# Kernel tuning notes

Measured on AMD Instinct MI355X. Metric: run time of the kernel, lower is better.

## Reference

```python
import jax, jax.numpy as jnp
import numpy as np

NQ = 64
BIG = 1e10

FILTERS = np.array([[1,0,0,1,0,0,1,0,0],
                    [0,0,0,0,0,0,1,1,1],
                    [0,0,1,0,0,1,0,0,1],
                    [1,1,1,0,0,0,0,0,0],
                    [0,0,0,1,0,0,1,1,0],
                    [0,0,0,0,0,1,0,1,1],
                    [0,1,1,0,0,1,0,0,0],
                    [1,1,0,1,0,0,0,0,0]], dtype=np.float32).reshape(8,1,3,3)


def _conv2d(x, k):
    return jax.lax.conv_general_dilated(x, k, (1,1), 'SAME',
                                        dimension_numbers=('NCHW','OIHW','NCHW'))


def _maxpool3(x):  # 3x3 stride-1 maxpool, pad=1 (pads with -inf like torch)
    return jax.lax.reduce_window(x, -jnp.inf, jax.lax.max, (1,1,3,3), (1,1,1,1), 'SAME')


def setup_inputs() -> dict:
    key = jax.random.key(0)
    ks = jax.random.split(key, 5)
    b, h, w = 2, 240, 320
    n = 2 * h * w  # 153600 points
    fx = fy = 300.0
    cx, cy = w / 2.0, h / 2.0
    z  = jax.random.uniform(ks[0], (b, n), minval=1.0, maxval=10.0)
    u  = jax.random.uniform(ks[1], (b, n), minval=0.0, maxval=float(w))
    v  = jax.random.uniform(ks[2], (b, n), minval=0.0, maxval=float(h))
    xw = (u - cx) / fx * z
    yw = (v - cy) / fy * z
    rgb = jax.random.uniform(ks[3], (b, 3, n))
    pp = jnp.concatenate([xw[:, None], yw[:, None], z[:, None],
                          jnp.ones((b, 1, n), jnp.float32), rgb], axis=1)  # [b,7,n]
    conf = jax.random.uniform(ks[4], (b, n))
    pose_w2c = jnp.tile(jnp.eye(4, dtype=jnp.float32)[None], (b, 1, 1))
    K = jnp.tile(jnp.array([[fx, 0, cx], [0, fy, cy], [0, 0, 1.0]], jnp.float32)[None], (b, 1, 1))
    filters = jnp.asarray(FILTERS)
    return {"pp": pp, "conf": conf, "pose_w2c": pose_w2c, "K": K,
            "filters": filters, "h": h, "w": w}


def reference(pp, conf, pose_w2c, K, filters, h, w,
              znear=0.1, zfar=1000.0, conf_thresh=0.0):
    b, _, n = pp.shape
    # world -> camera (wsz=1 so the hi-res pool is identity)
    pc = jnp.einsum('bij,bjn->bin', pose_w2c, pp[:, :4])          # [b,4,n]
    z  = jnp.abs(pc[:, 2])                                        # [b,n]
    xc = pc[:, 0] * K[:, 0, 0][:, None] / z + K[:, 0, 2][:, None]
    yc = pc[:, 1] * K[:, 1, 1][:, None] / z + K[:, 1, 2][:, None]
    x = jnp.round(xc).astype(jnp.int32)
    y = jnp.round(yc).astype(jnp.int32)
    oob = ((x < 0) | (x >= w) | (y < 0) | (y >= h) |
           (z < znear) | (z > zfar) | (conf <= conf_thresh))
    # inverse-depth quantization bounds over valid points only
    inv_lo = 1.0 / jnp.where(oob, 1e-10, z)   # oob -> 1e10, drops out of min
    inv_hi = 1.0 / jnp.where(oob, BIG, z)     # oob -> 1e-10, drops out of max
    dmin = jnp.min(inv_lo, axis=-1, keepdims=True)
    dmax = jnp.max(inv_hi, axis=-1, keepdims=True)
    do = ((inv_hi - dmin) / (dmax - dmin) * (NQ - 1)).astype(jnp.int32)  # [b,n]

    # scatter points into [b, NQ, h, w] z-buffer bins (drop invalid)
    size = b * NQ * h * w
    bidx = jnp.arange(b, dtype=jnp.int32)[:, None]
    idx = ((bidx * NQ + do) * h + y) * w + x
    idx = jnp.where(oob, size, idx).reshape(-1)   # 'size' is out of bounds -> dropped
    zf = z.astype(jnp.float32).reshape(-1)
    dmap = jnp.zeros((size,), jnp.float32).at[idx].set(zf, mode='drop').reshape(b, NQ, h, w)
    cmap = jnp.full((size,), -1.0, jnp.float32).at[idx].set(conf.reshape(-1), mode='drop').reshape(b, NQ, h, w)
    rgb_pts = pp[:, 4:].transpose(0, 2, 1).reshape(-1, 3).astype(jnp.float32)
    rgb = jnp.zeros((size, 3), jnp.float32).at[idx].set(rgb_pts, mode='drop').reshape(b, NQ, h, w, 3)

    # z-buffer composite: nearest non-empty bin per pixel
    dmap = jnp.where(dmap <= 0, BIG, dmap)
    min_idx = jnp.argmin(dmap, axis=1)                             # [b,h,w]
    dflat = jnp.min(dmap, axis=1)
    dflat = jnp.where(dflat >= BIG, 0.0, dflat)
    cflat = jnp.take_along_axis(cmap, min_idx[:, None], axis=1)[:, 0]
    cflat = jnp.maximum(cflat, 0.0)                                # cmap_[cmap_<0]=0
    rflat = jnp.take_along_axis(rgb, min_idx[:, None, :, :, None], axis=1)[:, 0]  # [b,h,w,3]

    # vertical flip (torch.flip over h)
    depths = dflat[:, ::-1][:, None]                               # [b,1,h,w]
    confs  = cflat[:, ::-1][:, None]
    rgbs   = jnp.transpose(rflat[:, ::-1], (0, 3, 1, 2))           # [b,3,h,w]

    # hole filling: 2 iterations of oriented-filter tests + 3x3 max pooling
    ones_k = jnp.ones((1, 1, 3, 3), jnp.float32)
    for _ in range(2):
        tofill = (_conv2d(depths, ones_k) > 0) & (depths <= 0)
        o = _conv2d(depths, filters)                               # [b,8,h,w]
        fill = (jnp.abs(jnp.prod(o, axis=1, keepdims=True)) > 1e-10) & tofill
        f = fill.astype(jnp.float32)
        depths = depths * (1 - f) + f * _maxpool3(depths)
        confs  = confs  * (1 - f) + f * _maxpool3(confs)
        rgbs   = rgbs   * (1 - f) + f * _maxpool3(rgbs)
    return depths, confs, rgbs
```

## Files before the change

### kernel.cpp

```cpp
#include <hip/hip_runtime.h>
#include <stdint.h>

#define NQ 64
#define ZNEAR 0.1f
#define ZFAR 1000.0f
#define FT 16

__device__ __forceinline__ float wave_min_f(float v) {
    #pragma unroll
    for (int off = 1; off < 64; off <<= 1)
        v = fminf(v, __shfl_xor(v, off, 64));
    return v;
}
__device__ __forceinline__ float wave_max_f(float v) {
    #pragma unroll
    for (int off = 1; off < 64; off <<= 1)
        v = fmaxf(v, __shfl_xor(v, off, 64));
    return v;
}

__global__ void k_project(const float* __restrict__ pp, const float* __restrict__ conf,
                          const float* __restrict__ pose, const float* __restrict__ Km,
                          const int* __restrict__ hp, const int* __restrict__ wp,
                          int B, int n,
                          float* __restrict__ zbuf, unsigned* __restrict__ packed,
                          float* __restrict__ pmin, float* __restrict__ pmax, int nBlk) {
    int bb = blockIdx.y;
    int i = blockIdx.x * blockDim.x + threadIdx.x;
    int h = *hp, w = *wp;
    float inv_lo = INFINITY;
    float inv_hi = 0.0f;
    if (i < n) {
        const float* P  = pose + (size_t)bb * 16;
        const float* km = Km   + (size_t)bb * 9;
        const float* pb = pp   + (size_t)bb * 7 * n;
        float X  = pb[0 * (size_t)n + i];
        float Y  = pb[1 * (size_t)n + i];
        float Z  = pb[2 * (size_t)n + i];
        float Wc = pb[3 * (size_t)n + i];
        float pc0 = P[0] * X + P[1] * Y + P[2]  * Z + P[3]  * Wc;
        float pc1 = P[4] * X + P[5] * Y + P[6]  * Z + P[7]  * Wc;
        float pc2 = P[8] * X + P[9] * Y + P[10] * Z + P[11] * Wc;
        float z = fabsf(pc2);
        float xc = pc0 * km[0] / z + km[2];
        float yc = pc1 * km[4] / z + km[5];
        float xr = rintf(xc);
        float yr = rintf(yc);
        float cf = conf[(size_t)bb * n + i];
        bool valid = (xr >= 0.0f) && (xr <= (float)(w - 1)) &&
                     (yr >= 0.0f) && (yr <= (float)(h - 1)) &&
                     (z >= ZNEAR) && (z <= ZFAR) && (cf > 0.0f);
        unsigned px = valid ? (unsigned)(int)xr : 0u;
        unsigned py = valid ? (unsigned)(int)yr : 0u;
        zbuf[(size_t)bb * n + i] = z;
        packed[(size_t)bb * n + i] = (valid ? 0x80000000u : 0u) | px | (py << 12);
        inv_lo = valid ? (1.0f / z) : (1.0f / 1e-10f);
        inv_hi = valid ? (1.0f / z) : (1.0f / 1e10f);
    }
    __shared__ float smin[4], smax[4];
    float wmin = wave_min_f(inv_lo);
    float wmax = wave_max_f(inv_hi);
    int lane = threadIdx.x & 63, wid = threadIdx.x >> 6;
    if (lane == 0) { smin[wid] = wmin; smax[wid] = wmax; }
    __syncthreads();
    if (threadIdx.x == 0) {
        pmin[(size_t)bb * nBlk + blockIdx.x] = fminf(fminf(smin[0], smin[1]), fminf(smin[2], smin[3]));
        pmax[(size_t)bb * nBlk + blockIdx.x] = fmaxf(fmaxf(smax[0], smax[1]), fmaxf(smax[2], smax[3]));
    }
}

__global__ void k_minmax(const float* __restrict__ pmin, const float* __restrict__ pmax,
                         int B, int nBlk, float* __restrict__ dminb, float* __restrict__ dmaxb) {
    __shared__ float smin[4], smax[4];
    for (int bb = 0; bb < B; ++bb) {
        float lmin = INFINITY, lmax = 0.0f;
        for (int k = threadIdx.x; k < nBlk; k += blockDim.x) {
            lmin = fminf(lmin, pmin[(size_t)bb * nBlk + k]);
            lmax = fmaxf(lmax, pmax[(size_t)bb * nBlk + k]);
        }
        lmin = wave_min_f(lmin);
        lmax = wave_max_f(lmax);
        int lane = threadIdx.x & 63, wid = threadIdx.x >> 6;
        if (lane == 0) { smin[wid] = lmin; smax[wid] = lmax; }
        __syncthreads();
        if (threadIdx.x == 0) {
            dminb[bb] = fminf(fminf(smin[0], smin[1]), fminf(smin[2], smin[3]));
            dmaxb[bb] = fmaxf(fmaxf(smax[0], smax[1]), fmaxf(smax[2], smax[3]));
        }
        __syncthreads();
    }
}

__global__ void k_scatter(const float* __restrict__ zbuf, const unsigned* __restrict__ packed,
                          const float* __restrict__ dminb, const float* __restrict__ dmaxb,
                          const int* __restrict__ hp, const int* __restrict__ wp,
                          int B, int n, unsigned* __restrict__ pixwin) {
    int p = blockIdx.x * blockDim.x + threadIdx.x;
    if (p >= B * n) return;
    unsigned pk = packed[p];
    if (!(pk & 0x80000000u)) return;
    int bb = p / n;
    int i = p - bb * n;
    float inv = 1.0f / zbuf[p];
    float dlo = dminb[bb], dhi = dmaxb[bb];
    int dq = (int)((inv - dlo) / (dhi - dlo) * (float)(NQ - 1));
    int h = *hp, w = *wp;
    int x = (int)(pk & 0xFFFu);
    int y = (int)((pk >> 12) & 0xFFFu);
    unsigned key = ((unsigned)dq << 20) | (unsigned)(i + 1);
    atomicMax(&pixwin[(size_t)bb * h * w + (size_t)y * w + x], key);
}

__global__ void k_resolve(const float* __restrict__ pp, const float* __restrict__ conf,
                          const float* __restrict__ zbuf, const unsigned* __restrict__ pixwin,
                          const int* __restrict__ hp, const int* __restrict__ wp,
                          int B, int n, float* __restrict__ field, int pixTot) {
    int q = blockIdx.x * blockDim.x + threadIdx.x;
    if (q >= pixTot) return;
    int h = *hp, w = *wp;
    int hw = h * w;
    int bb = q / hw;
    int rem = q - bb * hw;
    int y = rem / w;
    int x = rem - y * w;
    unsigned key = pixwin[q];
    float dz = 0.0f, dc = 0.0f, r0 = 0.0f, r1 = 0.0f, r2 = 0.0f;
    if (key) {
        int i = (int)(key & 0xFFFFFu) - 1;
        size_t p = (size_t)bb * n + i;
        dz = zbuf[p];
        dc = conf[p];
        r0 = pp[((size_t)bb * 7 + 4) * n + i];
        r1 = pp[((size_t)bb * 7 + 5) * n + i];
        r2 = pp[((size_t)bb * 7 + 6) * n + i];
    }
    int fy = h - 1 - y;
    size_t o = (size_t)bb * hw + (size_t)fy * w + x;
    field[o] = dz;
    field[(size_t)pixTot + o] = dc;
    size_t rb = 2 * (size_t)pixTot;
    field[rb + (((size_t)bb * 3 + 0) * h + fy) * w + x] = r0;
    field[rb + (((size_t)bb * 3 + 1) * h + fy) * w + x] = r1;
    field[rb + (((size_t)bb * 3 + 2) * h + fy) * w + x] = r2;
}

__global__ void k_fill2(const float* __restrict__ in, float* __restrict__ out,
                        const float* __restrict__ filt,
                        const int* __restrict__ hp, const int* __restrict__ wp,
                        int pixTot) {
    int h = *hp, w = *wp;
    int tilesX = (w + FT - 1) / FT;
    int tilesY = (h + FT - 1) / FT;
    int tile = blockIdx.x;
    if (tile >= tilesX * tilesY) return;
    int bb = blockIdx.y;
    int tY = tile / tilesX, tX = tile - tY * tilesX;
    int gy0 = tY * FT - 2, gx0 = tX * FT - 2;
    int hw = h * w;

    __shared__ float s_f[72];
    __shared__ float s_in[5][20][20];
    __shared__ float s_m[5][18][18];
    int tid = threadIdx.x;
    if (tid < 72) s_f[tid] = filt[tid];

    const float* base[5];
    base[0] = in + (size_t)bb * hw;
    base[1] = in + (size_t)pixTot + (size_t)bb * hw;
    base[2] = in + 2 * (size_t)pixTot + ((size_t)bb * 3 + 0) * hw;
    base[3] = in + 2 * (size_t)pixTot + ((size_t)bb * 3 + 1) * hw;
    base[4] = in + 2 * (size_t)pixTot + ((size_t)bb * 3 + 2) * hw;

    for (int idx = tid; idx < 400; idx += blockDim.x) {
        int yy = idx / 20, xx = idx - yy * 20;
        int gy = gy0 + yy, gx = gx0 + xx;
        bool v = ((unsigned)gy < (unsigned)h) && ((unsigned)gx < (unsigned)w);
        size_t g = (size_t)gy * w + gx;
        #pragma unroll
        for (int ch = 0; ch < 5; ++ch)
            s_in[ch][yy][xx] = v ? base[ch][g] : 0.0f;
    }
    __syncthreads();

    for (int idx = tid; idx < 324; idx += blockDim.x) {
        int py = idx / 18, px = idx - py * 18;
        int sy = py + 1, sx = px + 1;
        int gy = gy0 + sy, gx = gx0 + sx;
        bool vc = ((unsigned)gy < (unsigned)h) && ((unsigned)gx < (unsigned)w);
        float d[9];
        #pragma unroll
        for (int t = 0; t < 9; ++t) d[t] = s_in[0][sy + t / 3 - 1][sx + t % 3 - 1];
        float s = 0.0f;
        #pragma unroll
        for (int t = 0; t < 9; ++t) s += d[t];
        float dc0 = d[4];
        float ov[5];
        #pragma unroll
        for (int ch = 0; ch < 5; ++ch) ov[ch] = s_in[ch][sy][sx];
        if ((s > 0.0f) && (dc0 <= 0.0f)) {
            float prod = 1.0f;
            #pragma unroll
            for (int k = 0; k < 8; ++k) {
                float o = 0.0f;
                #pragma unroll
                for (int t = 0; t < 9; ++t) o += s_f[k * 9 + t] * d[t];
                prod *= o;
            }
            if (fabsf(prod) > 1e-10f) {
                #pragma unroll
                for (int ch = 0; ch < 5; ++ch) {
                    float m = -INFINITY;
                    #pragma unroll
                    for (int t = 0; t < 9; ++t) {
                        int ny = gy + t / 3 - 1, nx = gx + t % 3 - 1;
                        if (((unsigned)ny < (unsigned)h) && ((unsigned)nx < (unsigned)w))
                            m = fmaxf(m, s_in[ch][sy + t / 3 - 1][sx + t % 3 - 1]);
                    }
                    ov[ch] = m;
                }
            }
        }
        if (!vc) { ov[0] = 0.0f; ov[1] = 0.0f; ov[2] = 0.0f; ov[3] = 0.0f; ov[4] = 0.0f; }
        #pragma unroll
        for (int ch = 0; ch < 5; ++ch) s_m[ch][py][px] = ov[ch];
    }
    __syncthreads();

    int ly = tid >> 4, lx = tid & 15;
    int gy = tY * FT + ly, gx = tX * FT + lx;
    if (((unsigned)gy < (unsigned)h) && ((unsigned)gx < (unsigned)w)) {
        int sy = ly + 1, sx = lx + 1;
        float d[9];
        #pragma unroll
        for (int t = 0; t < 9; ++t) d[t] = s_m[0][sy + t / 3 - 1][sx + t % 3 - 1];
        float s = 0.0f;
        #pragma unroll
        for (int t = 0; t < 9; ++t) s += d[t];
        float dc0 = d[4];
        float ov[5];
        #pragma unroll
        for (int ch = 0; ch < 5; ++ch) ov[ch] = s_m[ch][sy][sx];
        if ((s > 0.0f) && (dc0 <= 0.0f)) {
            float prod = 1.0f;
            #pragma unroll
            for (int k = 0; k < 8; ++k) {
                float o = 0.0f;
                #pragma unroll
                for (int t = 0; t < 9; ++t) o += s_f[k * 9 + t] * d[t];
                prod *= o;
            }
            if (fabsf(prod) > 1e-10f) {
                #pragma unroll
                for (int ch = 0; ch < 5; ++ch) {
                    float m = -INFINITY;
                    #pragma unroll
                    for (int t = 0; t < 9; ++t) {
                        int ny = gy + t / 3 - 1, nx = gx + t % 3 - 1;
                        if (((unsigned)ny < (unsigned)h) && ((unsigned)nx < (unsigned)w))
                            m = fmaxf(m, s_m[ch][sy + t / 3 - 1][sx + t % 3 - 1]);
                    }
                    ov[ch] = m;
                }
            }
        }
        size_t g = (size_t)gy * w + gx;
        out[(size_t)bb * hw + g] = ov[0];
        out[(size_t)pixTot + (size_t)bb * hw + g] = ov[1];
        size_t rb = 2 * (size_t)pixTot;
        out[rb + (((size_t)bb * 3 + 0) * hw) + g] = ov[2];
        out[rb + (((size_t)bb * 3 + 1) * hw) + g] = ov[3];
        out[rb + (((size_t)bb * 3 + 2) * hw) + g] = ov[4];
    }
}

static inline size_t align16(size_t x) { return (x + 15) & ~(size_t)15; }

extern "C" void kernel_launch(void* const* d_in, const int* in_sizes, int n_in,
                              void* d_out, int out_size, void* d_ws, size_t ws_size,
                              hipStream_t stream) {
    const float* pp   = (const float*)d_in[0];
    const float* conf = (const float*)d_in[1];
    const float* pose = (const float*)d_in[2];
    const float* Km   = (const float*)d_in[3];
    const float* filt = (const float*)d_in[4];
    const int*   hp   = (const int*)d_in[5];
    const int*   wp   = (const int*)d_in[6];

    int B = in_sizes[2] / 16;
    int n = in_sizes[1] / B;
    size_t pix = (size_t)out_size / 5;
    size_t npts = (size_t)B * n;
    size_t hw = pix / B;

    const int bs = 256;
    int nBlk = (n + bs - 1) / bs;

    char* ws = (char*)d_ws;
    size_t off = 0;
    unsigned* pixwin = (unsigned*)(ws + off);  off = align16(off + pix * 4);
    float* zbuf   = (float*)(ws + off);        off = align16(off + npts * 4);
    unsigned* packed = (unsigned*)(ws + off);  off = align16(off + npts * 4);
    float* pminb  = (float*)(ws + off);        off = align16(off + (size_t)B * nBlk * 4);
    float* pmaxb  = (float*)(ws + off);        off = align16(off + (size_t)B * nBlk * 4);
    float* dminb  = (float*)(ws + off);        off = align16(off + (size_t)B * 4);
    float* dmaxb  = (float*)(ws + off);        off = align16(off + (size_t)B * 4);
    float* field  = (float*)(ws + off);        off = align16(off + (size_t)out_size * 4);

    float* out = (float*)d_out;

    hipMemsetAsync(pixwin, 0, pix * 4, stream);

    dim3 gproj(nBlk, B);
    k_project<<<gproj, bs, 0, stream>>>(pp, conf, pose, Km, hp, wp, B, n,
                                        zbuf, packed, pminb, pmaxb, nBlk);
    k_minmax<<<1, bs, 0, stream>>>(pminb, pmaxb, B, nBlk, dminb, dmaxb);

    int nptsI = (int)npts;
    k_scatter<<<(nptsI + bs - 1) / bs, bs, 0, stream>>>(zbuf, packed, dminb, dmaxb,
                                                        hp, wp, B, n, pixwin);
    int pixI = (int)pix;
    k_resolve<<<(pixI + bs - 1) / bs, bs, 0, stream>>>(pp, conf, zbuf, pixwin, hp, wp,
                                                       B, n, field, pixI);

    size_t tileBound = hw / (FT * FT) + hw / FT + 2;
    dim3 gfill((unsigned)tileBound, B);
    k_fill2<<<gfill, bs, 0, stream>>>(field, out, filt, hp, wp, pixI);
}
```

Baseline: 112.6 us.

## Fuse memset, minmax and resolve stages into neighbouring kernels

Clears pixwin inside the projection kernel in place of a separate memset. Folds the min/max reduction into every scatter block, so each block re-reduces the per-block partials. Packs conf and rgb into a float4 array during projection. The fill kernel now resolves the winning point per pixel itself, which removes the intermediate field buffer and two launches. In exchange, every scatter block repeats the small reduction, and the fill kernel does scattered gathers that include halo pixels.

```diff
diff --git a/kernel.cpp b/kernel.cpp
--- a/kernel.cpp
+++ b/kernel.cpp
@@ -24,9 +24,14 @@
                           const int* __restrict__ hp, const int* __restrict__ wp,
                           int B, int n,
                           float* __restrict__ zbuf, unsigned* __restrict__ packed,
-                          float* __restrict__ pmin, float* __restrict__ pmax, int nBlk) {
+                          float4* __restrict__ cr4,
+                          float* __restrict__ pmin, float* __restrict__ pmax, int nBlk,
+                          unsigned* __restrict__ pixwin, int pixTot) {
     int bb = blockIdx.y;
     int i = blockIdx.x * blockDim.x + threadIdx.x;
+    size_t ztid = ((size_t)blockIdx.y * gridDim.x + blockIdx.x) * blockDim.x + threadIdx.x;
+    if (ztid < (size_t)pixTot) pixwin[ztid] = 0u;
+
     int h = *hp, w = *wp;
     float inv_lo = INFINITY;
     float inv_hi = 0.0f;
@@ -52,8 +57,10 @@
                      (z >= ZNEAR) && (z <= ZFAR) && (cf > 0.0f);
         unsigned px = valid ? (unsigned)(int)xr : 0u;
         unsigned py = valid ? (unsigned)(int)yr : 0u;
-        zbuf[(size_t)bb * n + i] = z;
-        packed[(size_t)bb * n + i] = (valid ? 0x80000000u : 0u) | px | (py << 12);
+        size_t p = (size_t)bb * n + i;
+        zbuf[p] = z;
+        packed[p] = (valid ? 0x80000000u : 0u) | px | (py << 12);
+        cr4[p] = make_float4(cf, pb[4 * (size_t)n + i], pb[5 * (size_t)n + i], pb[6 * (size_t)n + i]);
         inv_lo = valid ? (1.0f / z) : (1.0f / 1e-10f);
         inv_hi = valid ? (1.0f / z) : (1.0f / 1e10f);
     }
@@ -69,14 +76,17 @@
     }
 }
 
-__global__ void k_minmax(const float* __restrict__ pmin, const float* __restrict__ pmax,
-                         int B, int nBlk, float* __restrict__ dminb, float* __restrict__ dmaxb) {
+__global__ void k_scatter(const float* __restrict__ zbuf, const unsigned* __restrict__ packed,
+                          const float* __restrict__ pminb, const float* __restrict__ pmaxb, int nBlk,
+                          const int* __restrict__ hp, const int* __restrict__ wp,
+                          int B, int n, unsigned* __restrict__ pixwin) {
     __shared__ float smin[4], smax[4];
+    __shared__ float sdlo[8], sdhi[8];
     for (int bb = 0; bb < B; ++bb) {
         float lmin = INFINITY, lmax = 0.0f;
         for (int k = threadIdx.x; k < nBlk; k += blockDim.x) {
-            lmin = fminf(lmin, pmin[(size_t)bb * nBlk + k]);
-            lmax = fmaxf(lmax, pmax[(size_t)bb * nBlk + k]);
+            lmin = fminf(lmin, pminb[(size_t)bb * nBlk + k]);
+            lmax = fmaxf(lmax, pmaxb[(size_t)bb * nBlk + k]);
         }
         lmin = wave_min_f(lmin);
         lmax = wave_max_f(lmax);
@@ -84,17 +94,11 @@
         if (lane == 0) { smin[wid] = lmin; smax[wid] = lmax; }
         __syncthreads();
         if (threadIdx.x == 0) {
-            dminb[bb] = fminf(fminf(smin[0], smin[1]), fminf(smin[2], smin[3]));
-            dmaxb[bb] = fmaxf(fmaxf(smax[0], smax[1]), fmaxf(smax[2], smax[3]));
+            sdlo[bb] = fminf(fminf(smin[0], smin[1]), fminf(smin[2], smin[3]));
+            sdhi[bb] = fmaxf(fmaxf(smax[0], smax[1]), fmaxf(smax[2], smax[3]));
         }
         __syncthreads();
     }
-}
-
-__global__ void k_scatter(const float* __restrict__ zbuf, const unsigned* __restrict__ packed,
-                          const float* __restrict__ dminb, const float* __restrict__ dmaxb,
-                          const int* __restrict__ hp, const int* __restrict__ wp,
-                          int B, int n, unsigned* __restrict__ pixwin) {
     int p = blockIdx.x * blockDim.x + threadIdx.x;
     if (p >= B * n) return;
     unsigned pk = packed[p];
@@ -102,7 +106,7 @@
     int bb = p / n;
     int i = p - bb * n;
     float inv = 1.0f / zbuf[p];
-    float dlo = dminb[bb], dhi = dmaxb[bb];
+    float dlo = sdlo[bb], dhi = sdhi[bb];
     int dq = (int)((inv - dlo) / (dhi - dlo) * (float)(NQ - 1));
     int h = *hp, w = *wp;
     int x = (int)(pk & 0xFFFu);
@@ -111,43 +115,11 @@
     atomicMax(&pixwin[(size_t)bb * h * w + (size_t)y * w + x], key);
 }
 
-__global__ void k_resolve(const float* __restrict__ pp, const float* __restrict__ conf,
-                          const float* __restrict__ zbuf, const unsigned* __restrict__ pixwin,
+__global__ void k_resfill(const float* __restrict__ zbuf, const float4* __restrict__ cr4,
+                          const unsigned* __restrict__ pixwin,
+                          const float* __restrict__ filt,
                           const int* __restrict__ hp, const int* __restrict__ wp,
-                          int B, int n, float* __restrict__ field, int pixTot) {
-    int q = blockIdx.x * blockDim.x + threadIdx.x;
-    if (q >= pixTot) return;
-    int h = *hp, w = *wp;
-    int hw = h * w;
-    int bb = q / hw;
-    int rem = q - bb * hw;
-    int y = rem / w;
-    int x = rem - y * w;
-    unsigned key = pixwin[q];
-    float dz = 0.0f, dc = 0.0f, r0 = 0.0f, r1 = 0.0f, r2 = 0.0f;
-    if (key) {
-        int i = (int)(key & 0xFFFFFu) - 1;
-        size_t p = (size_t)bb * n + i;
-        dz = zbuf[p];
-        dc = conf[p];
-        r0 = pp[((size_t)bb * 7 + 4) * n + i];
-        r1 = pp[((size_t)bb * 7 + 5) * n + i];
-        r2 = pp[((size_t)bb * 7 + 6) * n + i];
-    }
-    int fy = h - 1 - y;
-    size_t o = (size_t)bb * hw + (size_t)fy * w + x;
-    field[o] = dz;
-    field[(size_t)pixTot + o] = dc;
-    size_t rb = 2 * (size_t)pixTot;
-    field[rb + (((size_t)bb * 3 + 0) * h + fy) * w + x] = r0;
-    field[rb + (((size_t)bb * 3 + 1) * h + fy) * w + x] = r1;
-    field[rb + (((size_t)bb * 3 + 2) * h + fy) * w + x] = r2;
-}
-
-__global__ void k_fill2(const float* __restrict__ in, float* __restrict__ out,
-                        const float* __restrict__ filt,
-                        const int* __restrict__ hp, const int* __restrict__ wp,
-                        int pixTot) {
+                          int B, int n, float* __restrict__ out, int pixTot) {
     int h = *hp, w = *wp;
     int tilesX = (w + FT - 1) / FT;
     int tilesY = (h + FT - 1) / FT;
@@ -164,21 +136,26 @@
     int tid = threadIdx.x;
     if (tid < 72) s_f[tid] = filt[tid];
 
-    const float* base[5];
-    base[0] = in + (size_t)bb * hw;
-    base[1] = in + (size_t)pixTot + (size_t)bb * hw;
-    base[2] = in + 2 * (size_t)pixTot + ((size_t)bb * 3 + 0) * hw;
-    base[3] = in + 2 * (size_t)pixTot + ((size_t)bb * 3 + 1) * hw;
-    base[4] = in + 2 * (size_t)pixTot + ((size_t)bb * 3 + 2) * hw;
-
     for (int idx = tid; idx < 400; idx += blockDim.x) {
         int yy = idx / 20, xx = idx - yy * 20;
         int gy = gy0 + yy, gx = gx0 + xx;
-        bool v = ((unsigned)gy < (unsigned)h) && ((unsigned)gx < (unsigned)w);
-        size_t g = (size_t)gy * w + gx;
-        #pragma unroll
-        for (int ch = 0; ch < 5; ++ch)
-            s_in[ch][yy][xx] = v ? base[ch][g] : 0.0f;
+        float v0 = 0.0f, v1 = 0.0f, v2 = 0.0f, v3 = 0.0f, v4 = 0.0f;
+        if (((unsigned)gy < (unsigned)h) && ((unsigned)gx < (unsigned)w)) {
+            int ys = h - 1 - gy;
+            unsigned key = pixwin[(size_t)bb * hw + (size_t)ys * w + gx];
+            if (key) {
+                int i = (int)(key & 0xFFFFFu) - 1;
+                size_t p = (size_t)bb * n + i;
+                v0 = zbuf[p];
+                float4 cr = cr4[p];
+                v1 = cr.x; v2 = cr.y; v3 = cr.z; v4 = cr.w;
+            }
+        }
+        s_in[0][yy][xx] = v0;
+        s_in[1][yy][xx] = v1;
+        s_in[2][yy][xx] = v2;
+        s_in[3][yy][xx] = v3;
+        s_in[4][yy][xx] = v4;
     }
     __syncthreads();
 
@@ -300,29 +277,23 @@
     unsigned* pixwin = (unsigned*)(ws + off);  off = align16(off + pix * 4);
     float* zbuf   = (float*)(ws + off);        off = align16(off + npts * 4);
     unsigned* packed = (unsigned*)(ws + off);  off = align16(off + npts * 4);
+    float4* cr4   = (float4*)(ws + off);       off = align16(off + npts * 16);
     float* pminb  = (float*)(ws + off);        off = align16(off + (size_t)B * nBlk * 4);
     float* pmaxb  = (float*)(ws + off);        off = align16(off + (size_t)B * nBlk * 4);
-    float* dminb  = (float*)(ws + off);        off = align16(off + (size_t)B * 4);
-    float* dmaxb  = (float*)(ws + off);        off = align16(off + (size_t)B * 4);
-    float* field  = (float*)(ws + off);        off = align16(off + (size_t)out_size * 4);
 
     float* out = (float*)d_out;
-
-    hipMemsetAsync(pixwin, 0, pix * 4, stream);
+    int pixI = (int)pix;
 
     dim3 gproj(nBlk, B);
     k_project<<<gproj, bs, 0, stream>>>(pp, conf, pose, Km, hp, wp, B, n,
-                                        zbuf, packed, pminb, pmaxb, nBlk);
-    k_minmax<<<1, bs, 0, stream>>>(pminb, pmaxb, B, nBlk, dminb, dmaxb);
+                                        zbuf, packed, cr4, pminb, pmaxb, nBlk,
+                                        pixwin, pixI);
 
     int nptsI = (int)npts;
-    k_scatter<<<(nptsI + bs - 1) / bs, bs, 0, stream>>>(zbuf, packed, dminb, dmaxb,
+    k_scatter<<<(nptsI + bs - 1) / bs, bs, 0, stream>>>(zbuf, packed, pminb, pmaxb, nBlk,
                                                         hp, wp, B, n, pixwin);
-    int pixI = (int)pix;
-    k_resolve<<<(pixI + bs - 1) / bs, bs, 0, stream>>>(pp, conf, zbuf, pixwin, hp, wp,
-                                                       B, n, field, pixI);
 
     size_t tileBound = hw / (FT * FT) + hw / FT + 2;
     dim3 gfill((unsigned)tileBound, B);
-    k_fill2<<<gfill, bs, 0, stream>>>(field, out, filt, hp, wp, pixI);
-}
+    k_resfill<<<gfill, bs, 0, stream>>>(zbuf, cr4, pixwin, filt, hp, wp, B, n, out, pixI);
+}
```

New measurement: 104.7 us. 1.07x faster.
